# Performance work log

Hardware: AMD Instinct MI355X
Metric: run time of the kernel (lower is better)

Reference implementation:

```python
import jax, jax.numpy as jnp
import numpy as np

N_HEADS = 8
N_HIDDEN = 64  # out_features // n_heads
SLOPE = 0.2
NEG = -9e15


def setup_inputs() -> dict:
    key = jax.random.key(0)
    k1, k2, k3, k4, k5 = jax.random.split(key, 5)
    B, N, F_in, F_out = 4, 2048, 512, 512
    h = jax.random.normal(k1, (B, N, F_in), dtype=jnp.float32)
    adj = jax.random.randint(k2, (B, N, N), 0, 2, dtype=jnp.int32)
    # xavier_uniform with gain=1.414: limit = gain*sqrt(6/(fan_in+fan_out))
    lim_W = 1.414 * np.sqrt(6.0 / (F_in + F_out))
    W_l = jax.random.uniform(k3, (F_in, F_out), jnp.float32, -lim_W, lim_W)
    W_r = jax.random.uniform(k4, (F_in, F_out), jnp.float32, -lim_W, lim_W)
    lim_a = 1.414 * np.sqrt(6.0 / (N_HIDDEN + 1))
    a = jax.random.uniform(k5, (N_HIDDEN, 1), jnp.float32, -lim_a, lim_a)
    return {"h": h, "adj": adj, "W_l": W_l, "W_r": W_r, "a": a}


def reference(h, adj, W_l, W_r, a):
    B, N, _ = h.shape
    H, d = N_HEADS, N_HIDDEN
    # torch .view(-1, H, N, d) is a raw row-major reshape, replicated exactly here
    Wh_l = jax.nn.leaky_relu((h @ W_l).reshape(B, H, N, d), SLOPE)
    Wh_r = jax.nn.leaky_relu((h @ W_r).reshape(B, H, N, d), SLOPE)
    # e: [B,H,N,1] + [B,H,1,N] -> [B,H,N,N]
    e = Wh_l @ a + jnp.swapaxes(Wh_r @ a, 2, 3)
    att = jnp.where(adj[:, None, :, :] > 0, e, NEG)
    att = jax.nn.softmax(att, axis=-1)
    h_prime = att @ Wh_r  # [B,H,N,d]
    # torch .view(-1, N, H*d): raw reshape (no head transpose)
    out = jax.nn.elu(h_prime.reshape(B, N, H * d))
    return out
```

## Files before the change

kernel.cpp:

```cpp
#include <hip/hip_runtime.h>

#define NB   4
#define NN   2048
#define FIN  512
#define FOUT 512
#define NHD  8
#define DH   64
#define VTR  520
#define SLOPE 0.2f

typedef __attribute__((ext_vector_type(8)))  short bhalf8;
typedef __attribute__((ext_vector_type(16))) float f32x16;

__device__ __forceinline__ void load_lds16(const void* g, void* l) {
  __builtin_amdgcn_global_load_lds(
      (const __attribute__((address_space(1))) unsigned int*)g,
      (__attribute__((address_space(3))) unsigned int*)l, 16, 0, 0);
}

__device__ __forceinline__ unsigned short bfrne(float x) {
  unsigned int u = __float_as_uint(x);
  return (unsigned short)((u + 0x7FFFu + ((u >> 16) & 1u)) >> 16);
}

__device__ __forceinline__ void split2(float x, float y,
                                       unsigned int& hp, unsigned int& lp) {
  unsigned int ux = __float_as_uint(x), uy = __float_as_uint(y);
  unsigned int rx = (ux + 0x7FFFu + ((ux >> 16) & 1u)) & 0xFFFF0000u;
  unsigned int ry = (uy + 0x7FFFu + ((uy >> 16) & 1u)) & 0xFFFF0000u;
  float lx = x - __uint_as_float(rx);
  float ly = y - __uint_as_float(ry);
  unsigned int vx = __float_as_uint(lx), vy = __float_as_uint(ly);
  hp = (rx >> 16) | ry;
  lp = ((vx + 0x7FFFu + ((vx >> 16) & 1u)) >> 16)
     | ((vy + 0x7FFFu + ((vy >> 16) & 1u)) & 0xFFFF0000u);
}

__global__ __launch_bounds__(256) void k_split_prep(
    const float* __restrict__ h,
    unsigned short* __restrict__ hHi, unsigned short* __restrict__ hLo,
    const float* __restrict__ Wr,
    unsigned short* __restrict__ wTh, unsigned short* __restrict__ wTl)
{
  __shared__ float s[64][65];
  const int t = threadIdx.x;
  if (blockIdx.x < 2048) {
    size_t base = ((size_t)blockIdx.x * 256 + t) * 8;
    float4 a = *(const float4*)(h + base);
    float4 b = *(const float4*)(h + base + 4);
    uint4 uh, ul;
    split2(a.x, a.y, uh.x, ul.x);
    split2(a.z, a.w, uh.y, ul.y);
    split2(b.x, b.y, uh.z, ul.z);
    split2(b.z, b.w, uh.w, ul.w);
    *(uint4*)(hHi + base) = uh;
    *(uint4*)(hLo + base) = ul;
    return;
  }
  const int bid2 = blockIdx.x - 2048;
  const int n0 = (bid2 & 7) * 64, k0 = (bid2 >> 3) * 64;
#pragma unroll
  for (int p = 0; p < 4; ++p) {
    int row = p * 16 + (t >> 4);
    int col = (t & 15) * 4;
    float4 v = *(const float4*)(Wr + (size_t)(k0 + row) * FOUT + n0 + col);
    s[row][col] = v.x; s[row][col+1] = v.y; s[row][col+2] = v.z; s[row][col+3] = v.w;
  }
  __syncthreads();
  const int n = t >> 2;
  const int ks = (t & 3) * 16;
  uint4 h0, h1, l0, l1;
  split2(s[ks+ 0][n], s[ks+ 1][n], h0.x, l0.x);
  split2(s[ks+ 2][n], s[ks+ 3][n], h0.y, l0.y);
  split2(s[ks+ 4][n], s[ks+ 5][n], h0.z, l0.z);
  split2(s[ks+ 6][n], s[ks+ 7][n], h0.w, l0.w);
  split2(s[ks+ 8][n], s[ks+ 9][n], h1.x, l1.x);
  split2(s[ks+10][n], s[ks+11][n], h1.y, l1.y);
  split2(s[ks+12][n], s[ks+13][n], h1.z, l1.z);
  split2(s[ks+14][n], s[ks+15][n], h1.w, l1.w);
  size_t o = (size_t)(n0 + n) * FIN + k0 + ks;
  *(uint4*)(wTh + o) = h0; *(uint4*)(wTh + o + 8) = h1;
  *(uint4*)(wTl + o) = l0; *(uint4*)(wTl + o + 8) = l1;
}

__global__ __launch_bounds__(256) void k_gemm_whr_mfma(
    const unsigned short* __restrict__ hHi, const unsigned short* __restrict__ hLo,
    const unsigned short* __restrict__ wTh, const unsigned short* __restrict__ wTl,
    float* __restrict__ Whr, const float* __restrict__ av, float* __restrict__ er)
{
  __shared__ unsigned short sAh[128*64], sAl[128*64];
  __shared__ unsigned short sBh[64*64],  sBl[64*64];
  __shared__ float erT[128][2];
  const int tid = threadIdx.x, lane = tid & 63, wv = tid >> 6;
  const int Bid = blockIdx.x;
  const int g8 = Bid & 7, idx = Bid >> 3;
  const int sg = idx >> 3, ct = idx & 7;
  const int c0 = ct * 64;
  const int row0 = (g8 * 8 + sg) * 128;

  const unsigned short* pAh[4]; const unsigned short* pAl[4];
  unsigned short *dAh[4], *dAl[4];
#pragma unroll
  for (int t = 0; t < 4; ++t) {
    int I  = wv + t * 4;
    int rl = I * 8 + (lane >> 3);
    int gk = (lane & 7) ^ (rl & 7);
    pAh[t] = hHi + (size_t)(row0 + rl) * FIN + gk * 8;
    pAl[t] = hLo + (size_t)(row0 + rl) * FIN + gk * 8;
    dAh[t] = sAh + I * 512;  dAl[t] = sAl + I * 512;
  }
  const unsigned short* pBh[2]; const unsigned short* pBl[2];
  unsigned short *dBh[2], *dBl[2];
#pragma unroll
  for (int t = 0; t < 2; ++t) {
    int I  = wv + t * 4;
    int rl = I * 8 + (lane >> 3);
    int gk = (lane & 7) ^ (rl & 7);
    pBh[t] = wTh + (size_t)(c0 + rl) * FIN + gk * 8;
    pBl[t] = wTl + (size_t)(c0 + rl) * FIN + gk * 8;
    dBh[t] = sBh + I * 512;  dBl[t] = sBl + I * 512;
  }

  const int wi = wv >> 1, wc = wv & 1;
  const int l31 = lane & 31, half = lane >> 5;
  const int aoff0 = (wi*64 +      l31) * 64;
  const int aoff1 = (wi*64 + 32 + l31) * 64;
  const int boff  = (wc*32 +      l31) * 64;
  f32x16 acc0 = {}; f32x16 acc1 = {};

  for (int k0 = 0; k0 < FIN; k0 += 64) {
#pragma unroll
    for (int t = 0; t < 4; ++t) { load_lds16(pAh[t] + k0, dAh[t]);
                                  load_lds16(pAl[t] + k0, dAl[t]); }
#pragma unroll
    for (int t = 0; t < 2; ++t) { load_lds16(pBh[t] + k0, dBh[t]);
                                  load_lds16(pBl[t] + k0, dBl[t]); }
    __syncthreads();
#pragma unroll
    for (int kb = 0; kb < 4; ++kb) {
      int kg = ((kb*2 + half) ^ (lane & 7)) * 8;
      bhalf8 bh  = *(const bhalf8*)&sBh[boff  + kg];
      bhalf8 bl  = *(const bhalf8*)&sBl[boff  + kg];
      bhalf8 a0h = *(const bhalf8*)&sAh[aoff0 + kg];
      bhalf8 a0l = *(const bhalf8*)&sAl[aoff0 + kg];
      bhalf8 a1h = *(const bhalf8*)&sAh[aoff1 + kg];
      bhalf8 a1l = *(const bhalf8*)&sAl[aoff1 + kg];
      acc0 = __builtin_amdgcn_mfma_f32_32x32x16_bf16(a0h, bh, acc0, 0, 0, 0);
      acc1 = __builtin_amdgcn_mfma_f32_32x32x16_bf16(a1h, bh, acc1, 0, 0, 0);
      acc0 = __builtin_amdgcn_mfma_f32_32x32x16_bf16(a0l, bh, acc0, 0, 0, 0);
      acc1 = __builtin_amdgcn_mfma_f32_32x32x16_bf16(a1l, bh, acc1, 0, 0, 0);
      acc0 = __builtin_amdgcn_mfma_f32_32x32x16_bf16(a0h, bl, acc0, 0, 0, 0);
      acc1 = __builtin_amdgcn_mfma_f32_32x32x16_bf16(a1h, bl, acc1, 0, 0, 0);
    }
    __syncthreads();
  }

  const float a_d = av[wc*32 + l31];
#pragma unroll
  for (int mi = 0; mi < 2; ++mi) {
    const f32x16 a = mi ? acc1 : acc0;
#pragma unroll
    for (int reg = 0; reg < 16; ++reg) {
      int rmap = (reg & 3) + 8*(reg >> 2) + 4*half;
      int rowloc = wi*64 + mi*32 + rmap;
      int grow = row0 + rowloc;
      int b  = grow >> 11;
      int n  = grow & 2047;
      int hd = n >> 8;
      int jj = ((n & 255) << 3) | ct;
      float v = a[reg];
      v = v > 0.f ? v : SLOPE * v;
      Whr[(((size_t)(b*NHD + hd)) * NN + jj) * DH + (wc*32 + l31)] = v;
      float p = v * a_d;
      p += __shfl_xor(p, 16, 32);
      p += __shfl_xor(p,  8, 32);
      p += __shfl_xor(p,  4, 32);
      p += __shfl_xor(p,  2, 32);
      p += __shfl_xor(p,  1, 32);
      if (l31 == 0) erT[rowloc][wc] = p;
    }
  }
  __syncthreads();
  if (tid < 128) {
    int grow = row0 + tid;
    int b  = grow >> 11;
    int n  = grow & 2047;
    int hd = n >> 8;
    int jj = ((n & 255) << 3) | ct;
    er[((size_t)(b*NHD + hd)) * NN + jj] = erT[tid][0] + erT[tid][1];
  }
}

__global__ __launch_bounds__(256) void k_softvt(
    const float* __restrict__ Whr, const float* __restrict__ er,
    unsigned short* __restrict__ Vt)
{
  __shared__ float wm[4];
  __shared__ float wbuf[256];
  __shared__ unsigned short tile[64][264];
  const int tid = threadIdx.x;
  const int jc = blockIdx.x, hh = blockIdx.y, b = blockIdx.z;
  const float* ep = er + ((size_t)(b*NHD + hh)) * NN;
  float m = -1e30f;
  for (int j = tid; j < NN; j += 256) m = fmaxf(m, ep[j]);
#pragma unroll
  for (int off = 32; off; off >>= 1) m = fmaxf(m, __shfl_down(m, off, 64));
  if ((tid & 63) == 0) wm[tid >> 6] = m;
  __syncthreads();
  const float mm = fmaxf(fmaxf(wm[0], wm[1]), fmaxf(wm[2], wm[3]));
  const int j0 = jc * 256;
  float w = expf(ep[j0 + tid] - mm);
  wbuf[tid] = w;
  Vt[((size_t)(b*VTR + 512 + hh)) * NN + j0 + tid] = bfrne(w);
  __syncthreads();
  const size_t wbase = ((size_t)(b*NHD + hh)) * NN;
#pragma unroll
  for (int p = 0; p < 16; ++p) {
    int jr = p*16 + (tid >> 4);
    int dc = (tid & 15) * 4;
    float4 v = *(const float4*)(Whr + (wbase + j0 + jr) * DH + dc);
    float wj = wbuf[jr];
    tile[dc+0][jr] = bfrne(v.x * wj);
    tile[dc+1][jr] = bfrne(v.y * wj);
    tile[dc+2][jr] = bfrne(v.z * wj);
    tile[dc+3][jr] = bfrne(v.w * wj);
  }
  __syncthreads();
#pragma unroll
  for (int q = 0; q < 8; ++q) {
    int idx = q*256 + tid;
    int d = idx >> 5, seg = idx & 31;
    uint4 t16 = *(const uint4*)&tile[d][seg*8];
    *(uint4*)(Vt + ((size_t)(b*VTR + hh*64 + d)) * NN + j0 + seg*8) = t16;
  }
}

__global__ __launch_bounds__(256) void k_attn_out(
    const int* __restrict__ adj, const unsigned short* __restrict__ Vt,
    float* __restrict__ out)
{
  __shared__ unsigned short sA[128][72];
  __shared__ unsigned short sB[96][64];
  __shared__ float denL[128];
  const int tid = threadIdx.x;
  const int lane = tid & 63, wv = tid >> 6;
  const int Bid = blockIdx.x;
  const int g8 = Bid & 7, rest = Bid >> 3;
  const int ct = rest & 7, sg = rest >> 3;
  const int row0 = (g8*8 + sg) * 128;
  const int b = row0 >> 11;

  const unsigned short* pB[3];
  unsigned short* dB[3];
#pragma unroll
  for (int t = 0; t < 2; ++t) {
    int I  = wv + t*4;
    int rl = I*8 + (lane >> 3);
    int gk = (lane & 7) ^ (rl & 7);
    pB[t] = Vt + ((size_t)(b*VTR + ct*64 + rl))*NN + gk*8;
    dB[t] = &sB[0][0] + I*512;
  }
  {
    int x  = lane >> 3;
    int gk = (lane & 7) ^ (x & 7);
    pB[2] = Vt + ((size_t)(b*VTR + 512 + x))*NN + gk*8;
    dB[2] = &sB[0][0] + 8*512;
  }
  for (int idx = tid; idx < 384; idx += 256)
    ((uint4*)&sB[72][0])[idx] = uint4{0u,0u,0u,0u};

  const int* adjp = adj + (size_t)b*NN*NN + (size_t)(row0 & 2047)*NN
                    + (tid >> 3)*NN + (tid & 7)*8;
  unsigned short* sAp = &sA[tid >> 3][(tid & 7)*8];

  const int wi = wv >> 1, wc = wv & 1;
  const int l31 = lane & 31, half = lane >> 5;
  f32x16 acc0 = {}; f32x16 acc1 = {}; f32x16 acc2 = {};
  const unsigned short* aRd0 = &sA[wi*64 +      l31][half*8];
  const unsigned short* aRd1 = &sA[wi*64 + 32 + l31][half*8];
  const unsigned short* aRd2 = &sA[wv*32 +      l31][half*8];
  const int nloc = wc*32 + l31;

  for (int k0 = 0; k0 < NN; k0 += 64) {
    load_lds16(pB[0] + k0, dB[0]);
    load_lds16(pB[1] + k0, dB[1]);
    if (wv == 0) load_lds16(pB[2] + k0, dB[2]);
#pragma unroll
    for (int rr = 0; rr < 4; ++rr) {
      const int* p = adjp + rr*32*NN + k0;
      int4 q0 = *(const int4*)p;
      int4 q1 = *(const int4*)(p + 4);
      uint4 u;
      u.x = (unsigned)(q0.x | (q0.y << 16)) * 0x3F80u;
      u.y = (unsigned)(q0.z | (q0.w << 16)) * 0x3F80u;
      u.z = (unsigned)(q1.x | (q1.y << 16)) * 0x3F80u;
      u.w = (unsigned)(q1.z | (q1.w << 16)) * 0x3F80u;
      *(uint4*)(sAp + rr*32*72) = u;
    }
    __syncthreads();
#pragma unroll
    for (int kb = 0; kb < 4; ++kb) {
      int kg = (kb*2 + half) ^ (lane & 7);
      bhalf8 bf  = *(const bhalf8*)&sB[nloc][kg*8];
      bhalf8 bf2 = *(const bhalf8*)&sB[64 + l31][kg*8];
      bhalf8 a0 = *(const bhalf8*)(aRd0 + kb*16);
      bhalf8 a1 = *(const bhalf8*)(aRd1 + kb*16);
      bhalf8 a2 = *(const bhalf8*)(aRd2 + kb*16);
      acc0 = __builtin_amdgcn_mfma_f32_32x32x16_bf16(a0, bf,  acc0, 0, 0, 0);
      acc1 = __builtin_amdgcn_mfma_f32_32x32x16_bf16(a1, bf,  acc1, 0, 0, 0);
      acc2 = __builtin_amdgcn_mfma_f32_32x32x16_bf16(a2, bf2, acc2, 0, 0, 0);
    }
    __syncthreads();
  }
  if (l31 == ct) {
#pragma unroll
    for (int reg = 0; reg < 16; ++reg)
      denL[wv*32 + (reg & 3) + 8*(reg >> 2) + 4*half] = acc2[reg];
  }
  __syncthreads();
  const int ib = row0 & 2047;
#pragma unroll
  for (int mi = 0; mi < 2; ++mi) {
    const f32x16 a = mi ? acc1 : acc0;
#pragma unroll
    for (int reg = 0; reg < 16; ++reg) {
      int il = wi*64 + mi*32 + (reg & 3) + 8*(reg >> 2) + 4*half;
      int i  = ib + il;
      float v = a[reg] / denL[il];
      v = v > 0.f ? v : expm1f(v);
      int n = (ct << 8) | (i >> 3);
      int f = ((i & 7) << 6) | nloc;
      out[((size_t)b*NN + n)*FOUT + f] = v;
    }
  }
}

extern "C" void kernel_launch(void* const* d_in, const int* in_sizes, int n_in,
                              void* d_out, int out_size, void* d_ws, size_t ws_size,
                              hipStream_t stream)
{
  const float* hin = (const float*)d_in[0];
  const int*   adj = (const int*)d_in[1];
  const float* Wr  = (const float*)d_in[3];
  const float* av  = (const float*)d_in[4];
  float* out = (float*)d_out;

  char* ws = (char*)d_ws;
  unsigned short* hHi = (unsigned short*)(ws);
  unsigned short* hLo = (unsigned short*)(ws + 8388608);
  unsigned short* wTh = (unsigned short*)(ws + 16777216);
  unsigned short* wTl = (unsigned short*)(ws + 17301504);
  float* Whr  = (float*)(ws + 17825792);
  float* er   = (float*)(ws + 34603008);
  unsigned short* Vt = (unsigned short*)(ws);

  k_split_prep   <<<dim3(2112),    256, 0, stream>>>(hin, hHi, hLo, Wr, wTh, wTl);
  k_gemm_whr_mfma<<<dim3(512),     256, 0, stream>>>(hHi, hLo, wTh, wTl, Whr, av, er);
  k_softvt       <<<dim3(8, 8, 4), 256, 0, stream>>>(Whr, er, Vt);
  k_attn_out     <<<dim3(512),     256, 0, stream>>>(adj, Vt, out);
}
```

Before: 198.8 us.

## Double-buffer V tiles and register-prefetch adjacency in attention output kernel

The attention-output kernel now keeps two LDS buffers for the V tile. It issues the next iteration's global-to-LDS loads and adjacency int4 loads before the current MFMA block runs, so memory latency overlaps compute instead of sitting right before the barrier. It also drops the separate A-fragment read for the denominator MFMA by reusing a0/a1, since those cover the same rows. The padded zero rows of sB are no longer zero-filled; out-of-range lanes load a zero fragment instead. The cost is more LDS and more registers for the prefetched adjacency values, which may lower occupancy.

Result: no change. 198.6 us (-0.1%).

```diff
diff --git a/kernel.cpp b/kernel.cpp
--- a/kernel.cpp
+++ b/kernel.cpp
@@ -240,7 +240,7 @@
     float* __restrict__ out)
 {
   __shared__ unsigned short sA[128][72];
-  __shared__ unsigned short sB[96][64];
+  __shared__ unsigned short sB[2][72*64];
   __shared__ float denL[128];
   const int tid = threadIdx.x;
   const int lane = tid & 63, wv = tid >> 6;
@@ -251,23 +251,21 @@
   const int b = row0 >> 11;
 
   const unsigned short* pB[3];
-  unsigned short* dB[3];
+  int dOff[3];
 #pragma unroll
   for (int t = 0; t < 2; ++t) {
     int I  = wv + t*4;
     int rl = I*8 + (lane >> 3);
     int gk = (lane & 7) ^ (rl & 7);
     pB[t] = Vt + ((size_t)(b*VTR + ct*64 + rl))*NN + gk*8;
-    dB[t] = &sB[0][0] + I*512;
+    dOff[t] = I*512;
   }
   {
     int x  = lane >> 3;
     int gk = (lane & 7) ^ (x & 7);
     pB[2] = Vt + ((size_t)(b*VTR + 512 + x))*NN + gk*8;
-    dB[2] = &sB[0][0] + 8*512;
-  }
-  for (int idx = tid; idx < 384; idx += 256)
-    ((uint4*)&sB[72][0])[idx] = uint4{0u,0u,0u,0u};
+    dOff[2] = 64*64;
+  }
 
   const int* adjp = adj + (size_t)b*NN*NN + (size_t)(row0 & 2047)*NN
                     + (tid >> 3)*NN + (tid & 7)*8;
@@ -278,37 +276,54 @@
   f32x16 acc0 = {}; f32x16 acc1 = {}; f32x16 acc2 = {};
   const unsigned short* aRd0 = &sA[wi*64 +      l31][half*8];
   const unsigned short* aRd1 = &sA[wi*64 + 32 + l31][half*8];
-  const unsigned short* aRd2 = &sA[wv*32 +      l31][half*8];
   const int nloc = wc*32 + l31;
 
-  for (int k0 = 0; k0 < NN; k0 += 64) {
-    load_lds16(pB[0] + k0, dB[0]);
-    load_lds16(pB[1] + k0, dB[1]);
-    if (wv == 0) load_lds16(pB[2] + k0, dB[2]);
+  load_lds16(pB[0], &sB[0][dOff[0]]);
+  load_lds16(pB[1], &sB[0][dOff[1]]);
+  if (wv == 0) load_lds16(pB[2], &sB[0][dOff[2]]);
+  int4 q[8];
+#pragma unroll
+  for (int rr = 0; rr < 4; ++rr) {
+    q[2*rr]   = *(const int4*)(adjp + rr*32*NN);
+    q[2*rr+1] = *(const int4*)(adjp + rr*32*NN + 4);
+  }
+
+  for (int it = 0; it < 32; ++it) {
+    const int cur = it & 1;
 #pragma unroll
     for (int rr = 0; rr < 4; ++rr) {
-      const int* p = adjp + rr*32*NN + k0;
-      int4 q0 = *(const int4*)p;
-      int4 q1 = *(const int4*)(p + 4);
       uint4 u;
-      u.x = (unsigned)(q0.x | (q0.y << 16)) * 0x3F80u;
-      u.y = (unsigned)(q0.z | (q0.w << 16)) * 0x3F80u;
-      u.z = (unsigned)(q1.x | (q1.y << 16)) * 0x3F80u;
-      u.w = (unsigned)(q1.z | (q1.w << 16)) * 0x3F80u;
+      u.x = (unsigned)(q[2*rr].x   | (q[2*rr].y   << 16)) * 0x3F80u;
+      u.y = (unsigned)(q[2*rr].z   | (q[2*rr].w   << 16)) * 0x3F80u;
+      u.z = (unsigned)(q[2*rr+1].x | (q[2*rr+1].y << 16)) * 0x3F80u;
+      u.w = (unsigned)(q[2*rr+1].z | (q[2*rr+1].w << 16)) * 0x3F80u;
       *(uint4*)(sAp + rr*32*72) = u;
     }
     __syncthreads();
+    if (it < 31) {
+      const int nk = (it + 1) * 64;
+      unsigned short* nb = sB[cur ^ 1];
+      load_lds16(pB[0] + nk, nb + dOff[0]);
+      load_lds16(pB[1] + nk, nb + dOff[1]);
+      if (wv == 0) load_lds16(pB[2] + nk, nb + dOff[2]);
+#pragma unroll
+      for (int rr = 0; rr < 4; ++rr) {
+        q[2*rr]   = *(const int4*)(adjp + rr*32*NN + nk);
+        q[2*rr+1] = *(const int4*)(adjp + rr*32*NN + nk + 4);
+      }
+    }
+    const unsigned short* sBc = sB[cur];
 #pragma unroll
     for (int kb = 0; kb < 4; ++kb) {
       int kg = (kb*2 + half) ^ (lane & 7);
-      bhalf8 bf  = *(const bhalf8*)&sB[nloc][kg*8];
-      bhalf8 bf2 = *(const bhalf8*)&sB[64 + l31][kg*8];
+      bhalf8 bf  = *(const bhalf8*)&sBc[nloc*64 + kg*8];
+      bhalf8 bf2 = {};
+      if (l31 < 8) bf2 = *(const bhalf8*)&sBc[(64 + l31)*64 + kg*8];
       bhalf8 a0 = *(const bhalf8*)(aRd0 + kb*16);
       bhalf8 a1 = *(const bhalf8*)(aRd1 + kb*16);
-      bhalf8 a2 = *(const bhalf8*)(aRd2 + kb*16);
       acc0 = __builtin_amdgcn_mfma_f32_32x32x16_bf16(a0, bf,  acc0, 0, 0, 0);
       acc1 = __builtin_amdgcn_mfma_f32_32x32x16_bf16(a1, bf,  acc1, 0, 0, 0);
-      acc2 = __builtin_amdgcn_mfma_f32_32x32x16_bf16(a2, bf2, acc2, 0, 0, 0);
+      acc2 = __builtin_amdgcn_mfma_f32_32x32x16_bf16(wc ? a1 : a0, bf2, acc2, 0, 0, 0);
     }
     __syncthreads();
   }
```

## Widen attention tiles to two heads per block and store Whr as bf16

Applied to the files above, without the earlier changes.

The attention-output kernel now runs 512-thread blocks that each cover 128 value columns (two heads) instead of 64. This halves the number of times the int32 adjacency matrix is read and converted, which is the dominant memory traffic. The denominator MFMA is restricted to half the waves and keeps two per-head sums. Separately, the intermediate Whr tensor is stored as bf16 rather than fp32, halving that write and read; this adds one extra rounding step before the value is weighted.

Result: no change. 198.6 us (-0.1%).

```diff
diff --git a/kernel.cpp b/kernel.cpp
--- a/kernel.cpp
+++ b/kernel.cpp
@@ -21,6 +21,9 @@
 __device__ __forceinline__ unsigned short bfrne(float x) {
   unsigned int u = __float_as_uint(x);
   return (unsigned short)((u + 0x7FFFu + ((u >> 16) & 1u)) >> 16);
+}
+__device__ __forceinline__ float bf2f(unsigned short u) {
+  return __uint_as_float(((unsigned int)u) << 16);
 }
 
 __device__ __forceinline__ void split2(float x, float y,
@@ -86,7 +89,8 @@
 __global__ __launch_bounds__(256) void k_gemm_whr_mfma(
     const unsigned short* __restrict__ hHi, const unsigned short* __restrict__ hLo,
     const unsigned short* __restrict__ wTh, const unsigned short* __restrict__ wTl,
-    float* __restrict__ Whr, const float* __restrict__ av, float* __restrict__ er)
+    unsigned short* __restrict__ Whr, const float* __restrict__ av,
+    float* __restrict__ er)
 {
   __shared__ unsigned short sAh[128*64], sAl[128*64];
   __shared__ unsigned short sBh[64*64],  sBl[64*64];
@@ -170,7 +174,7 @@
       int jj = ((n & 255) << 3) | ct;
       float v = a[reg];
       v = v > 0.f ? v : SLOPE * v;
-      Whr[(((size_t)(b*NHD + hd)) * NN + jj) * DH + (wc*32 + l31)] = v;
+      Whr[(((size_t)(b*NHD + hd)) * NN + jj) * DH + (wc*32 + l31)] = bfrne(v);
       float p = v * a_d;
       p += __shfl_xor(p, 16, 32);
       p += __shfl_xor(p,  8, 32);
@@ -192,7 +196,7 @@
 }
 
 __global__ __launch_bounds__(256) void k_softvt(
-    const float* __restrict__ Whr, const float* __restrict__ er,
+    const unsigned short* __restrict__ Whr, const float* __restrict__ er,
     unsigned short* __restrict__ Vt)
 {
   __shared__ float wm[4];
@@ -218,12 +222,12 @@
   for (int p = 0; p < 16; ++p) {
     int jr = p*16 + (tid >> 4);
     int dc = (tid & 15) * 4;
-    float4 v = *(const float4*)(Whr + (wbase + j0 + jr) * DH + dc);
+    ushort4 v = *(const ushort4*)(Whr + (wbase + j0 + jr) * DH + dc);
     float wj = wbuf[jr];
-    tile[dc+0][jr] = bfrne(v.x * wj);
-    tile[dc+1][jr] = bfrne(v.y * wj);
-    tile[dc+2][jr] = bfrne(v.z * wj);
-    tile[dc+3][jr] = bfrne(v.w * wj);
+    tile[dc+0][jr] = bfrne(bf2f(v.x) * wj);
+    tile[dc+1][jr] = bfrne(bf2f(v.y) * wj);
+    tile[dc+2][jr] = bfrne(bf2f(v.z) * wj);
+    tile[dc+3][jr] = bfrne(bf2f(v.w) * wj);
   }
   __syncthreads();
 #pragma unroll
@@ -235,59 +239,50 @@
   }
 }
 
-__global__ __launch_bounds__(256) void k_attn_out(
+__global__ __launch_bounds__(512, 1) void k_attn_out(
     const int* __restrict__ adj, const unsigned short* __restrict__ Vt,
     float* __restrict__ out)
 {
   __shared__ unsigned short sA[128][72];
-  __shared__ unsigned short sB[96][64];
-  __shared__ float denL[128];
+  __shared__ unsigned short sB[136*64];
+  __shared__ float denL[128][2];
   const int tid = threadIdx.x;
   const int lane = tid & 63, wv = tid >> 6;
   const int Bid = blockIdx.x;
-  const int g8 = Bid & 7, rest = Bid >> 3;
-  const int ct = rest & 7, sg = rest >> 3;
+  const int g8 = Bid & 7, idx = Bid >> 3;
+  const int ctq = idx & 3, sg = idx >> 2;
   const int row0 = (g8*8 + sg) * 128;
   const int b = row0 >> 11;
 
-  const unsigned short* pB[3];
-  unsigned short* dB[3];
-#pragma unroll
-  for (int t = 0; t < 2; ++t) {
-    int I  = wv + t*4;
-    int rl = I*8 + (lane >> 3);
-    int gk = (lane & 7) ^ (rl & 7);
-    pB[t] = Vt + ((size_t)(b*VTR + ct*64 + rl))*NN + gk*8;
-    dB[t] = &sB[0][0] + I*512;
-  }
+  const unsigned short* pB0; const unsigned short* pB1; const unsigned short* pB2;
+  int dOff0, dOff1, dOff2;
   {
-    int x  = lane >> 3;
-    int gk = (lane & 7) ^ (x & 7);
-    pB[2] = Vt + ((size_t)(b*VTR + 512 + x))*NN + gk*8;
-    dB[2] = &sB[0][0] + 8*512;
-  }
-  for (int idx = tid; idx < 384; idx += 256)
-    ((uint4*)&sB[72][0])[idx] = uint4{0u,0u,0u,0u};
+    int I0 = wv,      rl0 = I0*8 + (lane >> 3), gk0 = (lane & 7) ^ (rl0 & 7);
+    int I1 = wv + 8,  rl1 = I1*8 + (lane >> 3), gk1 = (lane & 7) ^ (rl1 & 7);
+    pB0 = Vt + ((size_t)(b*VTR + ctq*128 + rl0))*NN + gk0*8;  dOff0 = I0*512;
+    pB1 = Vt + ((size_t)(b*VTR + ctq*128 + rl1))*NN + gk1*8;  dOff1 = I1*512;
+    int x = lane >> 3, gk2 = (lane & 7) ^ (x & 7);
+    pB2 = Vt + ((size_t)(b*VTR + 512 + x))*NN + gk2*8;        dOff2 = 16*512;
+  }
 
   const int* adjp = adj + (size_t)b*NN*NN + (size_t)(row0 & 2047)*NN
                     + (tid >> 3)*NN + (tid & 7)*8;
   unsigned short* sAp = &sA[tid >> 3][(tid & 7)*8];
 
-  const int wi = wv >> 1, wc = wv & 1;
+  const int wi = wv >> 2, wc = wv & 3;
   const int l31 = lane & 31, half = lane >> 5;
   f32x16 acc0 = {}; f32x16 acc1 = {}; f32x16 acc2 = {};
   const unsigned short* aRd0 = &sA[wi*64 +      l31][half*8];
   const unsigned short* aRd1 = &sA[wi*64 + 32 + l31][half*8];
-  const unsigned short* aRd2 = &sA[wv*32 +      l31][half*8];
-  const int nloc = wc*32 + l31;
+  const int boff = (wc*32 + l31) * 64;
 
   for (int k0 = 0; k0 < NN; k0 += 64) {
-    load_lds16(pB[0] + k0, dB[0]);
-    load_lds16(pB[1] + k0, dB[1]);
-    if (wv == 0) load_lds16(pB[2] + k0, dB[2]);
-#pragma unroll
-    for (int rr = 0; rr < 4; ++rr) {
-      const int* p = adjp + rr*32*NN + k0;
+    load_lds16(pB0 + k0, sB + dOff0);
+    load_lds16(pB1 + k0, sB + dOff1);
+    if (wv == 0) load_lds16(pB2 + k0, sB + dOff2);
+#pragma unroll
+    for (int rr = 0; rr < 2; ++rr) {
+      const int* p = adjp + rr*64*NN + k0;
       int4 q0 = *(const int4*)p;
       int4 q1 = *(const int4*)(p + 4);
       uint4 u;
@@ -295,30 +290,47 @@
       u.y = (unsigned)(q0.z | (q0.w << 16)) * 0x3F80u;
       u.z = (unsigned)(q1.x | (q1.y << 16)) * 0x3F80u;
       u.w = (unsigned)(q1.z | (q1.w << 16)) * 0x3F80u;
-      *(uint4*)(sAp + rr*32*72) = u;
+      *(uint4*)(sAp + rr*64*72) = u;
     }
     __syncthreads();
 #pragma unroll
     for (int kb = 0; kb < 4; ++kb) {
       int kg = (kb*2 + half) ^ (lane & 7);
-      bhalf8 bf  = *(const bhalf8*)&sB[nloc][kg*8];
-      bhalf8 bf2 = *(const bhalf8*)&sB[64 + l31][kg*8];
+      bhalf8 bf = *(const bhalf8*)&sB[boff + kg*8];
       bhalf8 a0 = *(const bhalf8*)(aRd0 + kb*16);
       bhalf8 a1 = *(const bhalf8*)(aRd1 + kb*16);
-      bhalf8 a2 = *(const bhalf8*)(aRd2 + kb*16);
-      acc0 = __builtin_amdgcn_mfma_f32_32x32x16_bf16(a0, bf,  acc0, 0, 0, 0);
-      acc1 = __builtin_amdgcn_mfma_f32_32x32x16_bf16(a1, bf,  acc1, 0, 0, 0);
-      acc2 = __builtin_amdgcn_mfma_f32_32x32x16_bf16(a2, bf2, acc2, 0, 0, 0);
+      acc0 = __builtin_amdgcn_mfma_f32_32x32x16_bf16(a0, bf, acc0, 0, 0, 0);
+      acc1 = __builtin_amdgcn_mfma_f32_32x32x16_bf16(a1, bf, acc1, 0, 0, 0);
+      if (wc < 2) {
+        bhalf8 bf2 = {};
+        if (l31 < 8) bf2 = *(const bhalf8*)&sB[(128 + l31)*64 + kg*8];
+        acc2 = __builtin_amdgcn_mfma_f32_32x32x16_bf16(wc ? a1 : a0, bf2, acc2, 0, 0, 0);
+      }
     }
     __syncthreads();
   }
-  if (l31 == ct) {
-#pragma unroll
-    for (int reg = 0; reg < 16; ++reg)
-      denL[wv*32 + (reg & 3) + 8*(reg >> 2) + 4*half] = acc2[reg];
-  }
-  __syncthreads();
+
+  const int hA = 2*ctq;
+  if (wc < 2) {
+    int rbase = wi*64 + wc*32;
+    if (l31 == hA) {
+#pragma unroll
+      for (int reg = 0; reg < 16; ++reg)
+        denL[rbase + (reg & 3) + 8*(reg >> 2) + 4*half][0] = acc2[reg];
+    }
+    if (l31 == hA + 1) {
+#pragma unroll
+      for (int reg = 0; reg < 16; ++reg)
+        denL[rbase + (reg & 3) + 8*(reg >> 2) + 4*half][1] = acc2[reg];
+    }
+  }
+  __syncthreads();
+
   const int ib = row0 & 2047;
+  const int c  = ctq*128 + wc*32 + l31;
+  const int d  = c & 63;
+  const int h  = c >> 6;
+  const int hloc = wc >> 1;
 #pragma unroll
   for (int mi = 0; mi < 2; ++mi) {
     const f32x16 a = mi ? acc1 : acc0;
@@ -326,10 +338,10 @@
     for (int reg = 0; reg < 16; ++reg) {
       int il = wi*64 + mi*32 + (reg & 3) + 8*(reg >> 2) + 4*half;
       int i  = ib + il;
-      float v = a[reg] / denL[il];
+      float v = a[reg] / denL[il][hloc];
       v = v > 0.f ? v : expm1f(v);
-      int n = (ct << 8) | (i >> 3);
-      int f = ((i & 7) << 6) | nloc;
+      int n = (h << 8) | (i >> 3);
+      int f = ((i & 7) << 6) | d;
       out[((size_t)b*NN + n)*FOUT + f] = v;
     }
   }
@@ -350,12 +362,12 @@
   unsigned short* hLo = (unsigned short*)(ws + 8388608);
   unsigned short* wTh = (unsigned short*)(ws + 16777216);
   unsigned short* wTl = (unsigned short*)(ws + 17301504);
-  float* Whr  = (float*)(ws + 17825792);
+  unsigned short* Whr = (unsigned short*)(ws + 17825792);
   float* er   = (float*)(ws + 34603008);
   unsigned short* Vt = (unsigned short*)(ws);
 
   k_split_prep   <<<dim3(2112),    256, 0, stream>>>(hin, hHi, hLo, Wr, wTh, wTl);
   k_gemm_whr_mfma<<<dim3(512),     256, 0, stream>>>(hHi, hLo, wTh, wTl, Whr, av, er);
   k_softvt       <<<dim3(8, 8, 4), 256, 0, stream>>>(Whr, er, Vt);
-  k_attn_out     <<<dim3(512),     256, 0, stream>>>(adj, Vt, out);
-}
+  k_attn_out     <<<dim3(256),     512, 0, stream>>>(adj, Vt, out);
+}
```
